# Optimization experiments

Hardware: AMD Instinct MI355X
Metric: run time of the kernel (lower is better)

The kernel has to match this reference:

```python
import jax, jax.numpy as jnp
import numpy as np

N = 50000          # nodes
E = 800000         # edges per view
B = 256            # graphs in batch
F = 128            # feature_dim
H, C = 2, 32       # GAT heads, out channels per head
NEG_SLOPE = 0.2    # PyG GATConv leaky_relu slope
EPS = 1e-5


def _gat_layer(h_in, src, dst, W, a_s, a_d, b):
    # h_in: [N, Fin]; W: [Fin, H*C]; a_s,a_d: [H,C]; b: [H*C]
    h = (h_in @ W).reshape(N, H, C)
    s_src = (h * a_s).sum(-1)                      # [N,H]
    s_dst = (h * a_d).sum(-1)                      # [N,H]
    e = jax.nn.leaky_relu(s_src[src] + s_dst[dst], NEG_SLOPE)   # [E',H]
    m = jax.ops.segment_max(e, dst, num_segments=N)
    p = jnp.exp(e - m[dst])
    z = jax.ops.segment_sum(p, dst, num_segments=N)
    w = p / z[dst]                                 # edge softmax over in-neighborhoods
    out = jax.ops.segment_sum(h[src] * w[:, :, None], dst, num_segments=N)
    return out.reshape(N, H * C) + b


def _encode_view(x, edge_index, batch, layer_params, ln_g, ln_b):
    # add self loops once (same edge_index each layer)
    loop = jnp.arange(N)
    src = jnp.concatenate([edge_index[0], loop])
    dst = jnp.concatenate([edge_index[1], loop])
    h = x
    hs = []
    for (W, a_s, a_d, b) in layer_params:
        h = jax.nn.elu(_gat_layer(h, src, dst, W, a_s, a_d, b))
        hs.append(h)
    h = jnp.concatenate(hs, axis=-1)               # [N,192] jumping knowledge
    mu = h.mean(-1, keepdims=True)
    var = ((h - mu) ** 2).mean(-1, keepdims=True)
    h = (h - mu) / jnp.sqrt(var + EPS) * ln_g + ln_b
    h_max = jax.ops.segment_max(h, batch, num_segments=B)
    cnt = jax.ops.segment_sum(jnp.ones((N, 1), h.dtype), batch, num_segments=B)
    h_mean = jax.ops.segment_sum(h, batch, num_segments=B) / jnp.maximum(cnt, 1.0)
    return jnp.concatenate([h_max, h_mean], axis=-1)   # [B,384]


def setup_inputs() -> dict:
    key = jax.random.key(0)
    ks = jax.random.split(key, 40)
    d = {}
    d['x'] = jax.random.normal(ks[0], (N, F), jnp.float32)
    d['edge_index_ast'] = jax.random.randint(ks[1], (2, E), 0, N)
    d['edge_index_cfg'] = jax.random.randint(ks[2], (2, E), 0, N)
    d['edge_index_pdg'] = jax.random.randint(ks[3], (2, E), 0, N)
    d['batch'] = jnp.sort(jax.random.randint(ks[4], (N,), 0, B))
    d['bn_gamma'] = jax.random.normal(ks[5], (F,), jnp.float32) * 0.1 + 1.0
    d['bn_beta'] = jax.random.normal(ks[6], (F,), jnp.float32) * 0.1
    ins = [F, H * C, H * C]
    i = 7
    for l in range(3):   # stacked over 3 views (ast,cfg,pdg)
        d[f'W{l}'] = jax.random.normal(ks[i], (3, ins[l], H * C), jnp.float32) * 0.1; i += 1
        d[f'as{l}'] = jax.random.normal(ks[i], (3, H, C), jnp.float32) * 0.1; i += 1
        d[f'ad{l}'] = jax.random.normal(ks[i], (3, H, C), jnp.float32) * 0.1; i += 1
        d[f'b{l}'] = jax.random.normal(ks[i], (3, H * C), jnp.float32) * 0.1; i += 1
    d['ln_gamma'] = jnp.ones((192,), jnp.float32)
    d['ln_beta'] = jnp.zeros((192,), jnp.float32)
    d['proj_W'] = jax.random.normal(ks[i], (384, 128), jnp.float32) * 0.05; i += 1
    d['proj_b'] = jnp.zeros((128,), jnp.float32)
    d['gW1'] = jax.random.normal(ks[i], (128, 64), jnp.float32) * 0.1; i += 1
    d['gb1'] = jnp.zeros((64,), jnp.float32)
    d['gW2'] = jax.random.normal(ks[i], (64, 3), jnp.float32) * 0.1; i += 1
    d['gb2'] = jnp.zeros((3,), jnp.float32)
    d['cW1'] = jax.random.normal(ks[i], (128, 128), jnp.float32) * 0.1; i += 1
    d['cb1'] = jnp.zeros((128,), jnp.float32)
    d['cW2'] = jax.random.normal(ks[i], (128, 64), jnp.float32) * 0.1; i += 1
    d['cb2'] = jnp.zeros((64,), jnp.float32)
    d['cW3'] = jax.random.normal(ks[i], (64, 1), jnp.float32) * 0.1; i += 1
    d['cb3'] = jnp.zeros((1,), jnp.float32)
    return d


def reference(x, edge_index_ast, edge_index_cfg, edge_index_pdg, batch,
              bn_gamma, bn_beta,
              W0, as0, ad0, b0, W1, as1, ad1, b1, W2, as2, ad2, b2,
              ln_gamma, ln_beta, proj_W, proj_b,
              gW1, gb1, gW2, gb2, cW1, cb1, cW2, cb2, cW3, cb3):
    # BatchNorm1d in eval mode: running_mean=0, running_var=1
    xn = x / jnp.sqrt(1.0 + EPS) * bn_gamma + bn_beta
    edges = [edge_index_ast, edge_index_cfg, edge_index_pdg]
    views = []
    for v in range(3):
        lp = [(W0[v], as0[v], ad0[v], b0[v]),
              (W1[v], as1[v], ad1[v], b1[v]),
              (W2[v], as2[v], ad2[v], b2[v])]
        hv = _encode_view(xn, edges[v], batch, lp, ln_gamma, ln_beta)  # [B,384]
        hv = jax.nn.relu(hv @ proj_W + proj_b)                          # shared view_proj
        views.append(hv)
    stacked = jnp.stack(views, axis=1)                                  # [B,3,128]
    gate_in = (views[0] + views[1] + views[2]) / 3.0
    alpha = jax.nn.softmax(jax.nn.relu(gate_in @ gW1 + gb1) @ gW2 + gb2, axis=-1)  # [B,3]
    fused = (stacked * alpha[:, :, None]).sum(axis=1)                   # [B,128]
    h = jax.nn.relu(fused @ cW1 + cb1)
    h = jax.nn.relu(h @ cW2 + cb2)
    logits = (h @ cW3 + cb3).squeeze(-1)                                # [B]
    return logits
```

## Files before the change

kernel.cpp:

```cpp
#include <hip/hip_runtime.h>
#include <math.h>

#define NN 50000
#define EE 800000
#define BB 256
#define FF 128
#define HC 64
#define NSLOPE 0.2f
#define EPSF 1e-5f
#define PK 8
#define CAP 48
#define NTILE ((NN + 15) / 16)
#define ECHUNKS (EE / 256)
#define NBK 100
#define BKN 500
#define SLOT 16

typedef _Float16 half4v __attribute__((ext_vector_type(4)));
typedef _Float16 half2v __attribute__((ext_vector_type(2)));
typedef _Float16 f16x8v __attribute__((ext_vector_type(8)));
typedef float f32x4v __attribute__((ext_vector_type(4)));

__global__ void k_sortA(const int* __restrict__ e0, const int* __restrict__ e1,
                        const int* __restrict__ e2, unsigned int* __restrict__ tmp) {
    __shared__ unsigned int stg[NBK][SLOT];
    __shared__ int lcnt[NBK];
    int tid = threadIdx.x;
    int v = blockIdx.y, bx = blockIdx.x;
    for (int i = tid; i < NBK; i += 256) lcnt[i] = 0;
    __syncthreads();
    int e = bx * 256 + tid;
    const int* ei = (v == 0) ? e0 : (v == 1) ? e1 : e2;
    int s = __builtin_nontemporal_load(ei + e);
    int d = __builtin_nontemporal_load(ei + EE + e);
    int bk = d / BKN;
    int dlo = d - bk * BKN;
    int idx = atomicAdd(&lcnt[bk], 1);
    if (idx < SLOT) stg[bk][idx] = (unsigned)s | ((unsigned)dlo << 16);
    __syncthreads();
    for (int i = tid; i < NBK * SLOT; i += 256) {
        int c = i >> 4, slot = i & 15;
        int n = min(lcnt[c], SLOT);
        long base = ((long)(v * NBK + c) * ECHUNKS + bx) * SLOT;
        tmp[base + slot] = (slot < n) ? stg[c][slot] : 0xFFFFFFFFu;
    }
}

__global__ __launch_bounds__(256)
void k_csrB(const unsigned int* __restrict__ tmp, int* __restrict__ cnt,
            unsigned short* __restrict__ col) {
    __shared__ unsigned short img[BKN * CAP];
    __shared__ int lcnt[BKN];
    int bi = blockIdx.x;
    int bk = bi % NBK;
    int v  = bi / NBK;
    int tid = threadIdx.x;
    for (int i = tid; i < BKN; i += 256) lcnt[i] = 0;
    __syncthreads();
    const unsigned int* stream = tmp + (long)(v * NBK + bk) * ECHUNKS * SLOT;
    const int total = ECHUNKS * SLOT;
    for (int base = 0; base < total; base += 2048) {
        unsigned int w[8];
#pragma unroll
        for (int k = 0; k < 8; ++k) {
            int i = base + k * 256 + tid;
            w[k] = (i < total) ? stream[i] : 0xFFFFFFFFu;
        }
#pragma unroll
        for (int k = 0; k < 8; ++k) {
            if (w[k] != 0xFFFFFFFFu) {
                int rel = (int)(w[k] >> 16);
                int idx = atomicAdd(&lcnt[rel], 1);
                if (idx < CAP) img[rel * CAP + idx] = (unsigned short)(w[k] & 0xFFFFu);
            }
        }
    }
    __syncthreads();
    int n0 = bk * BKN;
    unsigned int* gout = (unsigned int*)(col + ((long)v * NN + n0) * CAP);
    const unsigned int* gin = (const unsigned int*)img;
    for (int i = tid; i < BKN * CAP / 2; i += 256) gout[i] = gin[i];
    for (int i = tid; i < BKN; i += 256) cnt[v * NN + n0 + i] = lcnt[i];
}

__global__ void k_setup(const int* __restrict__ batch, int* __restrict__ bptr,
                        const float* __restrict__ W0, const float* __restrict__ W1,
                        const float* __restrict__ W2, _Float16* __restrict__ Wt,
                        const float* __restrict__ x, const float* __restrict__ bn_g,
                        const float* __restrict__ bn_b, _Float16* __restrict__ xh) {
    int b = blockIdx.x, tid = threadIdx.x;
    if (b < 196) {
        int n = b * 256 + tid;
        if (n >= NN) return;
        int bb = batch[n];
        int prev = (n == 0) ? -1 : batch[n - 1];
        for (int q = prev + 1; q <= bb; ++q) bptr[q] = n;
        if (n == NN - 1)
            for (int q = bb + 1; q <= BB; ++q) bptr[q] = NN;
    } else if (b < 205) {
        int id = b - 196;
        int v = id / 3, l = id - v * 3;
        int fin = (l == 0) ? 128 : 64;
        const float* src = ((l == 0) ? W0 : (l == 1) ? W1 : W2) + (long)v * fin * HC;
        _Float16* dst = Wt + (long)v * 16384 + ((l == 0) ? 0 : (l == 1) ? 8192 : 12288);
        for (int i = tid; i < fin * HC; i += 256) {
            int k = i >> 6, c = i & 63;
            dst[c * fin + k] = (_Float16)src[i];
        }
    } else {
        int i = (b - 205) * 256 + tid;
        if (i >= NN * 32) return;
        int base = i * 4;
        int k4 = base & 127;
        float4 xv = *(const float4*)&x[base];
        float4 gv = *(const float4*)&bn_g[k4];
        float4 bv = *(const float4*)&bn_b[k4];
        const float rsq = 1.0f / sqrtf(1.0f + EPSF);
        half4v o;
        o[0] = (_Float16)(xv.x * rsq * gv.x + bv.x);
        o[1] = (_Float16)(xv.y * rsq * gv.y + bv.y);
        o[2] = (_Float16)(xv.z * rsq * gv.z + bv.z);
        o[3] = (_Float16)(xv.w * rsq * gv.w + bv.w);
        *(half4v*)&xh[base] = o;
    }
}

template <int FIN, int INSTRIDE>
__global__ __launch_bounds__(256, 2)
void k_gemm_mfma(const _Float16* __restrict__ inp, long vstride, int in_off,
                 const _Float16* __restrict__ Wt, int wt_off,
                 const float* __restrict__ asl, const float* __restrict__ adl,
                 _Float16* __restrict__ h_lin, float* __restrict__ s_src,
                 float* __restrict__ s_dst) {
    const int NKT = FIN / 32;
    int gw = (blockIdx.x * 256 + threadIdx.x) >> 6;
    if (gw >= NTILE) return;
    int v = blockIdx.y;
    int lane = threadIdx.x & 63;
    int cn = lane & 15;
    int kg = lane >> 4;
    int n0 = gw << 4;

    const _Float16* wtv = Wt + (long)v * 16384 + wt_off;
    const float* a_s = asl + v * HC;
    const float* a_d = adl + v * HC;
    const _Float16* ipv = inp + (long)v * vstride + in_off;
    _Float16* hlv = h_lin + (long)v * NN * HC;
    float* ssv = s_src + (long)v * NN * 2;
    float* sdv = s_dst + (long)v * NN * 2;

    f16x8v bf[4][4];
#pragma unroll
    for (int t = 0; t < 4; ++t)
#pragma unroll
        for (int kt = 0; kt < NKT; ++kt)
            bf[t][kt] = *(const f16x8v*)&wtv[(t * 16 + cn) * FIN + kt * 32 + kg * 8];

    f32x4v acc[4];
#pragma unroll
    for (int t = 0; t < 4; ++t) acc[t] = (f32x4v){0.f, 0.f, 0.f, 0.f};

#pragma unroll
    for (int kt = 0; kt < NKT; ++kt) {
        f16x8v af = *(const f16x8v*)(ipv + (long)(n0 + cn) * INSTRIDE + kt * 32 + kg * 8);
#pragma unroll
        for (int t = 0; t < 4; ++t)
            acc[t] = __builtin_amdgcn_mfma_f32_16x16x32_f16(af, bf[t][kt], acc[t], 0, 0, 0);
    }

    float asv[4], adv[4];
#pragma unroll
    for (int t = 0; t < 4; ++t) {
        asv[t] = a_s[t * 16 + cn];
        adv[t] = a_d[t * 16 + cn];
    }
#pragma unroll
    for (int reg = 0; reg < 4; ++reg) {
        int n = n0 + kg * 4 + reg;
#pragma unroll
        for (int t = 0; t < 4; ++t)
            hlv[(long)n * HC + t * 16 + cn] = (_Float16)acc[t][reg];
        float ps0 = acc[0][reg] * asv[0] + acc[1][reg] * asv[1];
        float ps1 = acc[2][reg] * asv[2] + acc[3][reg] * asv[3];
        float pd0 = acc[0][reg] * adv[0] + acc[1][reg] * adv[1];
        float pd1 = acc[2][reg] * adv[2] + acc[3][reg] * adv[3];
#pragma unroll
        for (int msk = 8; msk >= 1; msk >>= 1) {
            ps0 += __shfl_xor(ps0, msk);
            ps1 += __shfl_xor(ps1, msk);
            pd0 += __shfl_xor(pd0, msk);
            pd1 += __shfl_xor(pd1, msk);
        }
        if (cn == 0) {
            ssv[n * 2]     = ps0;
            ssv[n * 2 + 1] = ps1;
            sdv[n * 2]     = pd0;
            sdv[n * 2 + 1] = pd1;
        }
    }
}

template <bool LAST>
__global__ void k_gat(const int* __restrict__ cnt, const unsigned short* __restrict__ col,
                      const float* __restrict__ s_src, const float* __restrict__ s_dst,
                      const _Float16* __restrict__ h_lin, const float* __restrict__ bl,
                      _Float16* __restrict__ hcat, int loff, float2* __restrict__ mu_inv) {
    int tid = threadIdx.x;
    int wid = blockIdx.x * 16 + (tid >> 4);
    int l16 = tid & 15;
    int gbase = (tid & 63) & ~15;
    if (wid >= NN) return;
    int v = blockIdx.y;
    const int* cv = cnt + (long)v * NN;
    const unsigned short* crow = col + ((long)v * NN + wid) * CAP;
    const float* ssv = s_src + (long)v * NN * 2;
    const float* sdv = s_dst + (long)v * NN * 2;
    const _Float16* hlv = h_lin + (long)v * NN * HC;
    const float* bias = bl + v * HC;
    _Float16* slice = hcat + (long)v * NN * 192 + loff;
    int cw = min(cv[wid], CAP);
    int nch = (cw + 15) >> 4;
    float sd0 = sdv[2 * wid], sd1 = sdv[2 * wid + 1];
    float2 ssw = *(const float2*)&ssv[2 * wid];
    float es0 = ssw.x + sd0, es1 = ssw.y + sd1;
    es0 = es0 > 0.0f ? es0 : NSLOPE * es0;
    es1 = es1 > 0.0f ? es1 : NSLOPE * es1;
    int c4 = l16 << 2;
    bool hd1 = c4 >= 32;

    int sv[3];
    float e0v[3], e1v[3];
#pragma unroll
    for (int c = 0; c < 3; ++c) {
        int i = c * 16 + l16;
        bool valid = i < cw;
        sv[c] = valid ? (int)crow[i] : 0;
        float e0 = -INFINITY, e1 = -INFINITY;
        if (valid) {
            float2 ss = *(const float2*)&ssv[2 * sv[c]];
            e0 = ss.x + sd0; e1 = ss.y + sd1;
            e0 = e0 > 0.0f ? e0 : NSLOPE * e0;
            e1 = e1 > 0.0f ? e1 : NSLOPE * e1;
        }
        e0v[c] = e0; e1v[c] = e1;
    }
    float m0 = fmaxf(e0v[0], fmaxf(e0v[1], e0v[2]));
    float m1 = fmaxf(e1v[0], fmaxf(e1v[1], e1v[2]));
#pragma unroll
    for (int msk = 8; msk >= 1; msk >>= 1) {
        m0 = fmaxf(m0, __shfl_xor(m0, msk));
        m1 = fmaxf(m1, __shfl_xor(m1, msk));
    }
    m0 = fmaxf(m0, es0);
    m1 = fmaxf(m1, es1);
    float z0 = 0.0f, z1 = 0.0f;
    int pki[3];
#pragma unroll
    for (int c = 0; c < 3; ++c) {
        float p0 = __expf(e0v[c] - m0);
        float p1 = __expf(e1v[c] - m1);
        z0 += p0; z1 += p1;
        half2v pk; pk[0] = (_Float16)p0; pk[1] = (_Float16)p1;
        pki[c] = *(int*)&pk;
    }
#pragma unroll
    for (int msk = 8; msk >= 1; msk >>= 1) {
        z0 += __shfl_xor(z0, msk);
        z1 += __shfl_xor(z1, msk);
    }
    float pself0 = __expf(es0 - m0), pself1 = __expf(es1 - m1);
    z0 += pself0;
    z1 += pself1;

    float pws = hd1 ? pself1 : pself0;
    const half4v hvs = *(const half4v*)&hlv[(long)wid * HC + c4];
    float4 t0, t1, t2, t3;
    t0.x = (float)hvs[0] * pws; t0.y = (float)hvs[1] * pws;
    t0.z = (float)hvs[2] * pws; t0.w = (float)hvs[3] * pws;
    t1 = make_float4(0.f, 0.f, 0.f, 0.f);
    t2 = make_float4(0.f, 0.f, 0.f, 0.f);
    t3 = make_float4(0.f, 0.f, 0.f, 0.f);
    for (int c = 0; c < nch; ++c) {
        int cend = min(16, cw - c * 16);
        int s = sv[c], pk = pki[c];
        int j = 0;
        for (; j + 4 <= cend; j += 4) {
            int sa = __shfl(s, gbase + j);
            int sb = __shfl(s, gbase + j + 1);
            int sc = __shfl(s, gbase + j + 2);
            int sd = __shfl(s, gbase + j + 3);
            int ua = __shfl(pk, gbase + j);
            int ub = __shfl(pk, gbase + j + 1);
            int uc = __shfl(pk, gbase + j + 2);
            int ud = __shfl(pk, gbase + j + 3);
            const half4v ha = *(const half4v*)&hlv[(long)sa * HC + c4];
            const half4v hb = *(const half4v*)&hlv[(long)sb * HC + c4];
            const half4v hc = *(const half4v*)&hlv[(long)sc * HC + c4];
            const half4v hd = *(const half4v*)&hlv[(long)sd * HC + c4];
            half2v pa = *(half2v*)&ua, pb = *(half2v*)&ub;
            half2v pc = *(half2v*)&uc, pd = *(half2v*)&ud;
            float wa = (float)(hd1 ? pa[1] : pa[0]);
            float wb = (float)(hd1 ? pb[1] : pb[0]);
            float wc = (float)(hd1 ? pc[1] : pc[0]);
            float wd = (float)(hd1 ? pd[1] : pd[0]);
            t0.x += (float)ha[0] * wa; t0.y += (float)ha[1] * wa;
            t0.z += (float)ha[2] * wa; t0.w += (float)ha[3] * wa;
            t1.x += (float)hb[0] * wb; t1.y += (float)hb[1] * wb;
            t1.z += (float)hb[2] * wb; t1.w += (float)hb[3] * wb;
            t2.x += (float)hc[0] * wc; t2.y += (float)hc[1] * wc;
            t2.z += (float)hc[2] * wc; t2.w += (float)hc[3] * wc;
            t3.x += (float)hd[0] * wd; t3.y += (float)hd[1] * wd;
            t3.z += (float)hd[2] * wd; t3.w += (float)hd[3] * wd;
        }
        for (; j < cend; ++j) {
            int sj = __shfl(s, gbase + j);
            int uj = __shfl(pk, gbase + j);
            half2v ph = *(half2v*)&uj;
            float pw = (float)(hd1 ? ph[1] : ph[0]);
            const half4v hv = *(const half4v*)&hlv[(long)sj * HC + c4];
            t0.x += (float)hv[0] * pw; t0.y += (float)hv[1] * pw;
            t0.z += (float)hv[2] * pw; t0.w += (float)hv[3] * pw;
        }
    }
    float zz = hd1 ? z1 : z0;
    float inv = 1.0f / zz;
    float4 b4 = *(const float4*)&bias[c4];
    float ox = ((t0.x + t1.x) + (t2.x + t3.x)) * inv + b4.x;
    float oy = ((t0.y + t1.y) + (t2.y + t3.y)) * inv + b4.y;
    float oz = ((t0.z + t1.z) + (t2.z + t3.z)) * inv + b4.z;
    float ow = ((t0.w + t1.w) + (t2.w + t3.w)) * inv + b4.w;
    ox = ox > 0.0f ? ox : __expf(ox) - 1.0f;
    oy = oy > 0.0f ? oy : __expf(oy) - 1.0f;
    oz = oz > 0.0f ? oz : __expf(oz) - 1.0f;
    ow = ow > 0.0f ? ow : __expf(ow) - 1.0f;
    half4v oh;
    oh[0] = (_Float16)ox; oh[1] = (_Float16)oy;
    oh[2] = (_Float16)oz; oh[3] = (_Float16)ow;
    *(half4v*)&slice[(long)wid * 192 + c4] = oh;

    if (LAST) {
        float sm = ox + oy + oz + ow;
        float sq = ox * ox + oy * oy + oz * oz + ow * ow;
        const _Float16* row = slice + (long)wid * 192 - 128;
        f16x8v rv = *(const f16x8v*)&row[l16 * 8];
#pragma unroll
        for (int j = 0; j < 8; ++j) {
            float u = (float)rv[j];
            sm += u; sq += u * u;
        }
#pragma unroll
        for (int msk = 8; msk >= 1; msk >>= 1) {
            sm += __shfl_xor(sm, msk);
            sq += __shfl_xor(sq, msk);
        }
        if (l16 == 0) {
            float mu  = sm * (1.0f / 192.0f);
            float var = sq * (1.0f / 192.0f) - mu * mu;
            mu_inv[(long)v * NN + wid] = make_float2(mu, 1.0f / sqrtf(var + EPSF));
        }
    }
}

__global__ void k_pool(const _Float16* __restrict__ hcat, const int* __restrict__ bptr,
                       const float2* __restrict__ mu_inv, const float* __restrict__ lng,
                       const float* __restrict__ lnb, float* __restrict__ part) {
    int v  = blockIdx.y;
    int b  = blockIdx.x >> 3;
    int kk = blockIdx.x & (PK - 1);
    int f  = threadIdx.x;
    const _Float16* hc = hcat + (long)v * NN * 192;
    const float2* mi = mu_inv + (long)v * NN;
    int s = bptr[b], e = bptr[b + 1];
    float g = lng[f], bo = lnb[f];
    float mx = -INFINITY, sm = 0.0f;
    for (int n = s + kk; n < e; n += PK) {
        float2 m = mi[n];
        float val = (float)hc[(long)n * 192 + f];
        float y = (val - m.x) * m.y * g + bo;
        mx = fmaxf(mx, y);
        sm += y;
    }
    long o = ((long)v * PK * BB + (long)kk * BB + b) * 384;
    part[o + f] = mx;
    part[o + 192 + f] = sm;
}

__global__ void k_proj(const float* __restrict__ part, const int* __restrict__ bptr,
                       const float* __restrict__ pW, const float* __restrict__ pb,
                       float* __restrict__ views) {
    __shared__ float pooled[384];
    int v = blockIdx.y;
    int b = blockIdx.x, tid = threadIdx.x;
    const float* pt = part + (long)v * PK * BB * 384;
    float invc = 1.0f / fmaxf((float)(bptr[b + 1] - bptr[b]), 1.0f);
    for (int i = tid; i < 384; i += 128) {
        bool ismax = i < 192;
        float acc = ismax ? -INFINITY : 0.0f;
        for (int kk = 0; kk < PK; ++kk) {
            float val = pt[((long)kk * BB + b) * 384 + i];
            acc = ismax ? fmaxf(acc, val) : (acc + val);
        }
        pooled[i] = ismax ? acc : acc * invc;
    }
    __syncthreads();
    float acc = pb[tid];
    for (int k = 0; k < 384; ++k) acc += pooled[k] * pW[k * 128 + tid];
    views[(long)v * BB * 128 + b * 128 + tid] = fmaxf(acc, 0.0f);
}

__global__ void k_final(const float* __restrict__ v0, const float* __restrict__ v1,
                        const float* __restrict__ v2,
                        const float* __restrict__ gW1, const float* __restrict__ gb1,
                        const float* __restrict__ gW2, const float* __restrict__ gb2,
                        const float* __restrict__ cW1, const float* __restrict__ cb1,
                        const float* __restrict__ cW2, const float* __restrict__ cb2,
                        const float* __restrict__ cW3, const float* __restrict__ cb3,
                        float* __restrict__ out) {
    __shared__ float gi[128], t1[64], alpha[3], fu[128], h1[128], h2[64];
    int b = blockIdx.x, tid = threadIdx.x;
    float a0 = v0[b * 128 + tid], a1 = v1[b * 128 + tid], a2 = v2[b * 128 + tid];
    gi[tid] = (a0 + a1 + a2) * (1.0f / 3.0f);
    __syncthreads();
    if (tid < 64) {
        float a = gb1[tid];
        for (int k = 0; k < 128; ++k) a += gi[k] * gW1[k * 64 + tid];
        t1[tid] = fmaxf(a, 0.0f);
    }
    __syncthreads();
    if (tid == 0) {
        float g[3];
        for (int j = 0; j < 3; ++j) {
            float a = gb2[j];
            for (int k = 0; k < 64; ++k) a += t1[k] * gW2[k * 3 + j];
            g[j] = a;
        }
        float mx = fmaxf(g[0], fmaxf(g[1], g[2]));
        float e0 = expf(g[0] - mx), e1 = expf(g[1] - mx), e2 = expf(g[2] - mx);
        float s = e0 + e1 + e2;
        alpha[0] = e0 / s; alpha[1] = e1 / s; alpha[2] = e2 / s;
    }
    __syncthreads();
    fu[tid] = alpha[0] * a0 + alpha[1] * a1 + alpha[2] * a2;
    __syncthreads();
    float a = cb1[tid];
    for (int k = 0; k < 128; ++k) a += fu[k] * cW1[k * 128 + tid];
    h1[tid] = fmaxf(a, 0.0f);
    __syncthreads();
    if (tid < 64) {
        float b2 = cb2[tid];
        for (int k = 0; k < 128; ++k) b2 += h1[k] * cW2[k * 64 + tid];
        h2[tid] = fmaxf(b2, 0.0f);
    }
    __syncthreads();
    if (tid == 0) {
        float a3 = cb3[0];
        for (int k = 0; k < 64; ++k) a3 += h2[k] * cW3[k];
        out[b] = a3;
    }
}

extern "C" void kernel_launch(void* const* d_in, const int* in_sizes, int n_in,
                              void* d_out, int out_size, void* d_ws, size_t ws_size,
                              hipStream_t stream) {
    const float* x     = (const float*)d_in[0];
    const int*   ei0   = (const int*)d_in[1];
    const int*   ei1   = (const int*)d_in[2];
    const int*   ei2   = (const int*)d_in[3];
    const int*   batch = (const int*)d_in[4];
    const float* bn_g  = (const float*)d_in[5];
    const float* bn_b  = (const float*)d_in[6];
    const float* W0  = (const float*)d_in[7];
    const float* W1  = (const float*)d_in[11];
    const float* W2  = (const float*)d_in[15];
    const float* asl[3] = {(const float*)d_in[8],  (const float*)d_in[12], (const float*)d_in[16]};
    const float* adl[3] = {(const float*)d_in[9],  (const float*)d_in[13], (const float*)d_in[17]};
    const float* bl[3]  = {(const float*)d_in[10], (const float*)d_in[14], (const float*)d_in[18]};
    const float* lng = (const float*)d_in[19];
    const float* lnb = (const float*)d_in[20];
    const float* pW  = (const float*)d_in[21];
    const float* pb  = (const float*)d_in[22];
    const float* gW1 = (const float*)d_in[23];
    const float* gb1 = (const float*)d_in[24];
    const float* gW2 = (const float*)d_in[25];
    const float* gb2 = (const float*)d_in[26];
    const float* cW1 = (const float*)d_in[27];
    const float* cb1 = (const float*)d_in[28];
    const float* cW2 = (const float*)d_in[29];
    const float* cb2 = (const float*)d_in[30];
    const float* cW3 = (const float*)d_in[31];
    const float* cb3 = (const float*)d_in[32];

    float* ws = (float*)d_ws;
    float* wt_f   = ws;
    _Float16* Wt  = (_Float16*)wt_f;
    int* bptr     = (int*)(wt_f + 24576);
    int* cnt      = bptr + 258;
    float* s_src  = (float*)(cnt + 3 * NN);
    float* s_dst  = s_src + 3 * NN * 2;
    float* mu_inv = s_dst + 3 * NN * 2;
    float* xh_f   = mu_inv + 3 * NN * 2;
    _Float16* xh  = (_Float16*)xh_f;
    unsigned short* col = (unsigned short*)(xh_f + (long)NN * 64);
    float* main_f = (float*)(col + (long)3 * NN * CAP);
    long mo = ((long)(main_f - ws) + 3) & ~3L;
    main_f = ws + mo;
    _Float16* hcat  = (_Float16*)main_f;
    float* hl_f     = main_f + (long)3 * NN * 96;
    _Float16* h_lin = (_Float16*)hl_f;
    float* part     = hl_f + (long)3 * NN * 32;
    float* views    = part + (long)3 * PK * BB * 384;
    unsigned int* tmp = (unsigned int*)main_f;

    k_setup<<<205 + (NN * 32 + 255) / 256, 256, 0, stream>>>(
        batch, bptr, W0, W1, W2, Wt, x, bn_g, bn_b, xh);
    k_sortA<<<dim3(ECHUNKS, 3), 256, 0, stream>>>(ei0, ei1, ei2, tmp);
    k_csrB<<<3 * NBK, 256, 0, stream>>>(tmp, cnt, col);

    const int GB = (NTILE * 64 + 255) / 256;

    k_gemm_mfma<128, 128><<<dim3(GB, 3), 256, 0, stream>>>(
        xh, 0, 0, Wt, 0, asl[0], adl[0], h_lin, s_src, s_dst);
    k_gat<false><<<dim3((NN + 15) / 16, 3), 256, 0, stream>>>(
        cnt, col, s_src, s_dst, h_lin, bl[0], hcat, 0, (float2*)mu_inv);
    k_gemm_mfma<64, 192><<<dim3(GB, 3), 256, 0, stream>>>(
        hcat, (long)NN * 192, 0, Wt, 8192, asl[1], adl[1], h_lin, s_src, s_dst);
    k_gat<false><<<dim3((NN + 15) / 16, 3), 256, 0, stream>>>(
        cnt, col, s_src, s_dst, h_lin, bl[1], hcat, HC, (float2*)mu_inv);
    k_gemm_mfma<64, 192><<<dim3(GB, 3), 256, 0, stream>>>(
        hcat, (long)NN * 192, HC, Wt, 12288, asl[2], adl[2], h_lin, s_src, s_dst);
    k_gat<true><<<dim3((NN + 15) / 16, 3), 256, 0, stream>>>(
        cnt, col, s_src, s_dst, h_lin, bl[2], hcat, 2 * HC, (float2*)mu_inv);

    k_pool<<<dim3(BB * PK, 3), 192, 0, stream>>>(hcat, bptr, (const float2*)mu_inv,
                                                 lng, lnb, part);
    k_proj<<<dim3(BB, 3), 128, 0, stream>>>(part, bptr, pW, pb, views);
    k_final<<<BB, 128, 0, stream>>>(views, views + BB * 128, views + 2 * BB * 128,
                                    gW1, gb1, gW2, gb2, cW1, cb1, cW2, cb2, cW3, cb3,
                                    (float*)d_out);
}
```

Baseline: 400.3 us.

## Use nontemporal loads/stores and fuse projection with final gating head

Switches streaming loads and stores in the GEMM, GAT and pooling kernels to nontemporal builtins, so streamed data is less likely to pollute cache. Separately, k_proj and k_final are merged into one 384-thread kernel per graph that computes all three view projections in shared memory and then runs the gate and classifier. This removes one launch and the global round-trip for the views buffer. The risk is that nontemporal hints hurt reuse of hcat rows that are read again later, and that most threads sit idle during the tail MLP.

Result: slower. 440.4 us (+10.0%).

```diff
diff --git a/kernel.cpp b/kernel.cpp
--- a/kernel.cpp
+++ b/kernel.cpp
@@ -162,7 +162,8 @@
 
 #pragma unroll
     for (int kt = 0; kt < NKT; ++kt) {
-        f16x8v af = *(const f16x8v*)(ipv + (long)(n0 + cn) * INSTRIDE + kt * 32 + kg * 8);
+        f16x8v af = __builtin_nontemporal_load(
+            (const f16x8v*)(ipv + (long)(n0 + cn) * INSTRIDE + kt * 32 + kg * 8));
 #pragma unroll
         for (int t = 0; t < 4; ++t)
             acc[t] = __builtin_amdgcn_mfma_f32_16x16x32_f16(af, bf[t][kt], acc[t], 0, 0, 0);
@@ -234,7 +235,7 @@
     for (int c = 0; c < 3; ++c) {
         int i = c * 16 + l16;
         bool valid = i < cw;
-        sv[c] = valid ? (int)crow[i] : 0;
+        sv[c] = valid ? (int)__builtin_nontemporal_load(crow + i) : 0;
         float e0 = -INFINITY, e1 = -INFINITY;
         if (valid) {
             float2 ss = *(const float2*)&ssv[2 * sv[c]];
@@ -336,7 +337,7 @@
     half4v oh;
     oh[0] = (_Float16)ox; oh[1] = (_Float16)oy;
     oh[2] = (_Float16)oz; oh[3] = (_Float16)ow;
-    *(half4v*)&slice[(long)wid * 192 + c4] = oh;
+    __builtin_nontemporal_store(oh, (half4v*)&slice[(long)wid * 192 + c4]);
 
     if (LAST) {
         float sm = ox + oy + oz + ow;
@@ -375,7 +376,7 @@
     float mx = -INFINITY, sm = 0.0f;
     for (int n = s + kk; n < e; n += PK) {
         float2 m = mi[n];
-        float val = (float)hc[(long)n * 192 + f];
+        float val = (float)__builtin_nontemporal_load(hc + (long)n * 192 + f);
         float y = (val - m.x) * m.y * g + bo;
         mx = fmaxf(mx, y);
         sm += y;
@@ -385,46 +386,43 @@
     part[o + 192 + f] = sm;
 }
 
-__global__ void k_proj(const float* __restrict__ part, const int* __restrict__ bptr,
-                       const float* __restrict__ pW, const float* __restrict__ pb,
-                       float* __restrict__ views) {
-    __shared__ float pooled[384];
-    int v = blockIdx.y;
-    int b = blockIdx.x, tid = threadIdx.x;
+__global__ void k_projfinal(const float* __restrict__ part, const int* __restrict__ bptr,
+                            const float* __restrict__ pW, const float* __restrict__ pb,
+                            const float* __restrict__ gW1, const float* __restrict__ gb1,
+                            const float* __restrict__ gW2, const float* __restrict__ gb2,
+                            const float* __restrict__ cW1, const float* __restrict__ cb1,
+                            const float* __restrict__ cW2, const float* __restrict__ cb2,
+                            const float* __restrict__ cW3, const float* __restrict__ cb3,
+                            float* __restrict__ out) {
+    __shared__ float pooled[3][384];
+    __shared__ float vv[3][128];
+    __shared__ float gi[128], t1[64], alpha[3], fu[128], h1[128], h2[64];
+    int b = blockIdx.x;
+    int tid = threadIdx.x;
+    int v = tid >> 7, t = tid & 127;
+    float invc = 1.0f / fmaxf((float)(bptr[b + 1] - bptr[b]), 1.0f);
     const float* pt = part + (long)v * PK * BB * 384;
-    float invc = 1.0f / fmaxf((float)(bptr[b + 1] - bptr[b]), 1.0f);
-    for (int i = tid; i < 384; i += 128) {
+    for (int i = t; i < 384; i += 128) {
         bool ismax = i < 192;
         float acc = ismax ? -INFINITY : 0.0f;
         for (int kk = 0; kk < PK; ++kk) {
             float val = pt[((long)kk * BB + b) * 384 + i];
             acc = ismax ? fmaxf(acc, val) : (acc + val);
         }
-        pooled[i] = ismax ? acc : acc * invc;
-    }
-    __syncthreads();
-    float acc = pb[tid];
-    for (int k = 0; k < 384; ++k) acc += pooled[k] * pW[k * 128 + tid];
-    views[(long)v * BB * 128 + b * 128 + tid] = fmaxf(acc, 0.0f);
-}
-
-__global__ void k_final(const float* __restrict__ v0, const float* __restrict__ v1,
-                        const float* __restrict__ v2,
-                        const float* __restrict__ gW1, const float* __restrict__ gb1,
-                        const float* __restrict__ gW2, const float* __restrict__ gb2,
-                        const float* __restrict__ cW1, const float* __restrict__ cb1,
-                        const float* __restrict__ cW2, const float* __restrict__ cb2,
-                        const float* __restrict__ cW3, const float* __restrict__ cb3,
-                        float* __restrict__ out) {
-    __shared__ float gi[128], t1[64], alpha[3], fu[128], h1[128], h2[64];
-    int b = blockIdx.x, tid = threadIdx.x;
-    float a0 = v0[b * 128 + tid], a1 = v1[b * 128 + tid], a2 = v2[b * 128 + tid];
-    gi[tid] = (a0 + a1 + a2) * (1.0f / 3.0f);
-    __syncthreads();
-    if (tid < 64) {
-        float a = gb1[tid];
-        for (int k = 0; k < 128; ++k) a += gi[k] * gW1[k * 64 + tid];
-        t1[tid] = fmaxf(a, 0.0f);
+        pooled[v][i] = ismax ? acc : acc * invc;
+    }
+    __syncthreads();
+    float acc = pb[t];
+    for (int k = 0; k < 384; ++k) acc += pooled[v][k] * pW[k * 128 + t];
+    vv[v][t] = fmaxf(acc, 0.0f);
+    __syncthreads();
+    if (v == 0)
+        gi[t] = (vv[0][t] + vv[1][t] + vv[2][t]) * (1.0f / 3.0f);
+    __syncthreads();
+    if (v == 0 && t < 64) {
+        float a = gb1[t];
+        for (int k = 0; k < 128; ++k) a += gi[k] * gW1[k * 64 + t];
+        t1[t] = fmaxf(a, 0.0f);
     }
     __syncthreads();
     if (tid == 0) {
@@ -440,16 +438,19 @@
         alpha[0] = e0 / s; alpha[1] = e1 / s; alpha[2] = e2 / s;
     }
     __syncthreads();
-    fu[tid] = alpha[0] * a0 + alpha[1] * a1 + alpha[2] * a2;
-    __syncthreads();
-    float a = cb1[tid];
-    for (int k = 0; k < 128; ++k) a += fu[k] * cW1[k * 128 + tid];
-    h1[tid] = fmaxf(a, 0.0f);
-    __syncthreads();
-    if (tid < 64) {
-        float b2 = cb2[tid];
-        for (int k = 0; k < 128; ++k) b2 += h1[k] * cW2[k * 64 + tid];
-        h2[tid] = fmaxf(b2, 0.0f);
+    if (v == 0)
+        fu[t] = alpha[0] * vv[0][t] + alpha[1] * vv[1][t] + alpha[2] * vv[2][t];
+    __syncthreads();
+    if (v == 0) {
+        float a = cb1[t];
+        for (int k = 0; k < 128; ++k) a += fu[k] * cW1[k * 128 + t];
+        h1[t] = fmaxf(a, 0.0f);
+    }
+    __syncthreads();
+    if (v == 0 && t < 64) {
+        float b2 = cb2[t];
+        for (int k = 0; k < 128; ++k) b2 += h1[k] * cW2[k * 64 + t];
+        h2[t] = fmaxf(b2, 0.0f);
     }
     __syncthreads();
     if (tid == 0) {
@@ -508,7 +509,6 @@
     float* hl_f     = main_f + (long)3 * NN * 96;
     _Float16* h_lin = (_Float16*)hl_f;
     float* part     = hl_f + (long)3 * NN * 32;
-    float* views    = part + (long)3 * PK * BB * 384;
     unsigned int* tmp = (unsigned int*)main_f;
 
     k_setup<<<205 + (NN * 32 + 255) / 256, 256, 0, stream>>>(
@@ -533,8 +533,7 @@
 
     k_pool<<<dim3(BB * PK, 3), 192, 0, stream>>>(hcat, bptr, (const float2*)mu_inv,
                                                  lng, lnb, part);
-    k_proj<<<dim3(BB, 3), 128, 0, stream>>>(part, bptr, pW, pb, views);
-    k_final<<<BB, 128, 0, stream>>>(views, views + BB * 128, views + 2 * BB * 128,
-                                    gW1, gb1, gW2, gb2, cW1, cb1, cW2, cb2, cW3, cb3,
-                                    (float*)d_out);
-}
+    k_projfinal<<<BB, 384, 0, stream>>>(part, bptr, pW, pb,
+                                        gW1, gb1, gW2, gb2, cW1, cb1, cW2, cb2,
+                                        cW3, cb3, (float*)d_out);
+}
```
